# Performance work log

Hardware: AMD Instinct MI355X
Metric: run time of the kernel (lower is better)

The kernel has to match this reference:

```python
import jax, jax.numpy as jnp
import numpy as np

L = 16384      # number of nodes / target positions
N = 1          # batch (graph batches are folded into one graph)
E = 512        # embed_dim
H = 8          # num_heads
D = E // H     # head_dim
DEG = 16       # avg in-degree per query node
NNZ = L * DEG  # number of edges


def setup_inputs() -> dict:
    key = jax.random.key(0)
    ks = jax.random.split(key, 8)
    query = jax.random.normal(ks[0], (L, N, E), dtype=jnp.float32)
    k_in = jax.random.normal(ks[1], (L, N, E), dtype=jnp.float32)
    v_in = jax.random.normal(ks[2], (L, N, E), dtype=jnp.float32)
    # edge list: each query node attends to DEG random source nodes
    row = jnp.repeat(jnp.arange(L, dtype=jnp.int64), DEG)            # (NNZ,)
    col = jax.random.randint(ks[3], (NNZ,), 0, L).astype(jnp.int64)  # (NNZ,)
    indices = jnp.stack([row, col], axis=0)                          # (2, NNZ)
    # parameters (xavier-uniform-like scale)
    in_proj_weight = jax.random.normal(ks[4], (3 * E, E), dtype=jnp.float32) * (1.0 / np.sqrt(E))
    in_proj_bias = jnp.zeros((3 * E,), dtype=jnp.float32)
    out_proj_weight = jax.random.normal(ks[5], (E, E), dtype=jnp.float32) * (1.0 / np.sqrt(E))
    out_proj_bias = jnp.zeros((E,), dtype=jnp.float32)
    return {
        "query": query, "key": k_in, "value": v_in, "indices": indices,
        "in_proj_weight": in_proj_weight, "in_proj_bias": in_proj_bias,
        "out_proj_weight": out_proj_weight, "out_proj_bias": out_proj_bias,
    }


def reference(query, key, value, indices, in_proj_weight, in_proj_bias,
              out_proj_weight, out_proj_bias):
    # QKV projections (in_proj_weight packs [Wq; Wk; Wv] row-wise, torch Linear convention)
    w_q, w_k, w_v = jnp.split(in_proj_weight, 3, axis=0)
    b_q, b_k, b_v = jnp.split(in_proj_bias, 3)
    scaling = 1.0 / jnp.sqrt(jnp.asarray(D, dtype=query.dtype))
    q = (query @ w_q.T + b_q) * scaling          # (L, N, E)
    k = key @ w_k.T + b_k                        # (L, N, E)
    v = value @ w_v.T + b_v                      # (L, N, E)
    # split heads: (L, N*H, D)
    q = q.reshape(L, N * H, D)
    k = k.reshape(L, N * H, D)
    v = v.reshape(L, N * H, D)

    row, col = indices[0], indices[1]
    qe = q[row]                                  # (NNZ, NH, D)
    ke = k[col]                                  # (NNZ, NH, D)
    scores = jnp.einsum('ehd,ehd->eh', qe, ke)   # (NNZ, NH)

    # segment softmax over each query node's edge set
    smax = jax.ops.segment_max(scores, row, num_segments=L)          # (L, NH)
    smax = jnp.where(jnp.isfinite(smax), smax, 0.0)                  # empty-segment guard
    expw = jnp.exp(scores - smax[row])                               # (NNZ, NH)
    denom = jax.ops.segment_sum(expw, row, num_segments=L)           # (L, NH)
    denom = jnp.where(denom > 0, denom, 1.0)
    attn = expw / denom[row]                                         # (NNZ, NH)

    # aggregate values along edges
    ve = v[col]                                                      # (NNZ, NH, D)
    out = jax.ops.segment_sum(attn[:, :, None] * ve, row, num_segments=L)  # (L, NH, D)
    out = out.reshape(L, N, E)
    # output projection
    return out @ out_proj_weight.T + out_proj_bias                   # (L, N, E)
```

## Files before the change

kernel.cpp:

```cpp
#include <hip/hip_runtime.h>
#include <math.h>

#define L_NODES 16384
#define EMB 512
#define NHEAD 8
#define HDIM 64
#define DEG 16
#define NNZ_E (L_NODES * DEG)

typedef __attribute__((ext_vector_type(8))) short short8;
typedef __attribute__((ext_vector_type(4))) float f32x4;

__device__ inline short f2bs(float x) {
    union { float f; unsigned u; } c; c.f = x;
    unsigned r = (c.u + 0x7fffu + ((c.u >> 16) & 1u)) >> 16;
    return (short)r;
}

__device__ inline void cv8(const float* __restrict__ s, short* __restrict__ d, int i) {
    float4 a = reinterpret_cast<const float4*>(s)[2 * i];
    float4 b = reinterpret_cast<const float4*>(s)[2 * i + 1];
    short8 o;
    o[0] = f2bs(a.x); o[1] = f2bs(a.y); o[2] = f2bs(a.z); o[3] = f2bs(a.w);
    o[4] = f2bs(b.x); o[5] = f2bs(b.y); o[6] = f2bs(b.z); o[7] = f2bs(b.w);
    reinterpret_cast<short8*>(d)[i] = o;
}

__global__ __launch_bounds__(256) void f2bw(
    const float* __restrict__ w1, short* __restrict__ d1, int n1,
    const float* __restrict__ w2, short* __restrict__ d2, int n2) {
    const int stride = gridDim.x * blockDim.x;
    for (int i = blockIdx.x * blockDim.x + threadIdx.x; i < n1 + n2; i += stride) {
        if (i < n1) cv8(w1, d1, i); else cv8(w2, d2, i - n1);
    }
}

__device__ inline void b2f8(short8 s, float* f) {
    const unsigned* u = reinterpret_cast<const unsigned*>(&s);
#pragma unroll
    for (int j = 0; j < 4; ++j) {
        unsigned lo = u[j] << 16;
        unsigned hi = u[j] & 0xFFFF0000u;
        f[2 * j]     = __builtin_bit_cast(float, lo);
        f[2 * j + 1] = __builtin_bit_cast(float, hi);
    }
}

__device__ inline void gload16(const short* g, short* l) {
    __builtin_amdgcn_global_load_lds(
        (const __attribute__((address_space(1))) unsigned*)g,
        (__attribute__((address_space(3))) unsigned*)l, 16, 0, 0);
}

__device__ inline short8 cvt16(float4 a0, float4 a1) {
    short8 s;
    s[0] = f2bs(a0.x); s[1] = f2bs(a0.y); s[2] = f2bs(a0.z); s[3] = f2bs(a0.w);
    s[4] = f2bs(a1.x); s[5] = f2bs(a1.y); s[6] = f2bs(a1.z); s[7] = f2bs(a1.w);
    return s;
}

__device__ inline int swz8(int r) { return ((r >> 1) & 3) | ((r & 1) << 2); }

#define QBM 128
#define QBN 256
#define QBK 64

__global__ __launch_bounds__(512) void gemm_qkv(
    const float* __restrict__ q_in, const float* __restrict__ k_in,
    const float* __restrict__ v_in, const short* __restrict__ wqkv,
    const float* __restrict__ bias_all,
    short* __restrict__ qo, short* __restrict__ ko, short* __restrict__ vo)
{
    __shared__ __align__(16) short As[QBM * QBK];
    __shared__ __align__(16) short Bs[QBN * QBK];

    const int gid   = blockIdx.x;
    const int which = gid >> 8;
    const int inner = gid & 255;

    const float* A    = which == 0 ? q_in : (which == 1 ? k_in : v_in);
    const short* B    = wqkv + which * 262144;
    const float* bias = bias_all + which * 512;
    short*       C    = which == 0 ? qo : (which == 1 ? ko : vo);
    const float scale = which == 0 ? 0.125f : 1.0f;

    const int t    = threadIdx.x;
    const int wid  = t >> 6;
    const int lane = t & 63;

    const int wg = (inner & 7) * 32 + (inner >> 3);
    const int bx = wg & 1;
    const int by = wg >> 1;
    const int row0 = by * QBM;
    const int col0 = bx * QBN;

    const int ar  = t >> 2;
    const int q2  = (t & 3) << 1;
    const int xa  = swz8(ar);
    const int p0  = q2 ^ xa;
    const int p1  = p0 ^ 1;
    const float* Aga = A + (size_t)(row0 + ar) * 512 + q2 * 8;
    short* awp0 = &As[ar * QBK + p0 * 8];
    short* awp1 = &As[ar * QBK + p1 * 8];

    const int brw = t >> 3;
    const int bp  = t & 7;
    const int xb  = swz8(brw & 7);
    const short* Bgb = B + (size_t)(col0 + brw) * 512 + (bp ^ xb) * 8;
    short* Bld = &Bs[(wid * 8) * QBK];

    const int wr = wid >> 2;
    const int wc = wid & 3;

    f32x4 acc[4][4] = {};

    for (int k0 = 0; k0 < 512; k0 += QBK) {
#pragma unroll
        for (int j = 0; j < 4; ++j)
            gload16(Bgb + (size_t)j * 64 * 512 + k0, Bld + j * 64 * QBK);
        {
            const float* ap = Aga + k0;
            float4 a0 = *reinterpret_cast<const float4*>(ap);
            float4 a1 = *reinterpret_cast<const float4*>(ap + 4);
            float4 a2 = *reinterpret_cast<const float4*>(ap + 8);
            float4 a3 = *reinterpret_cast<const float4*>(ap + 12);
            *reinterpret_cast<short8*>(awp0) = cvt16(a0, a1);
            *reinterpret_cast<short8*>(awp1) = cvt16(a2, a3);
        }
        __syncthreads();

#pragma unroll
        for (int kk = 0; kk < 2; ++kk) {
            short8 af[4], bf[4];
#pragma unroll
            for (int i = 0; i < 4; ++i) {
                const int r  = wr * 64 + i * 16 + (lane & 15);
                const int sl = (kk * 4 + (lane >> 4)) ^ swz8(r);
                af[i] = *reinterpret_cast<const short8*>(&As[r * QBK + sl * 8]);
            }
#pragma unroll
            for (int j = 0; j < 4; ++j) {
                const int r  = wc * 64 + j * 16 + (lane & 15);
                const int sl = (kk * 4 + (lane >> 4)) ^ swz8(r);
                bf[j] = *reinterpret_cast<const short8*>(&Bs[r * QBK + sl * 8]);
            }
#pragma unroll
            for (int i = 0; i < 4; ++i)
#pragma unroll
                for (int j = 0; j < 4; ++j)
                    acc[i][j] = __builtin_amdgcn_mfma_f32_16x16x32_bf16(
                        af[i], bf[j], acc[i][j], 0, 0, 0);
        }
        __syncthreads();
    }

    float bv[4];
#pragma unroll
    for (int j = 0; j < 4; ++j) bv[j] = bias[col0 + wc * 64 + j * 16 + (lane & 15)];
#pragma unroll
    for (int i = 0; i < 4; ++i) {
        const int rbase = row0 + wr * 64 + i * 16 + (lane >> 4) * 4;
#pragma unroll
        for (int j = 0; j < 4; ++j) {
            const int col = col0 + wc * 64 + j * 16 + (lane & 15);
#pragma unroll
            for (int rg = 0; rg < 4; ++rg)
                C[(size_t)(rbase + rg) * 512 + col] =
                    f2bs((acc[i][j][rg] + bv[j]) * scale);
        }
    }
}

#define OBK 64

__global__ __launch_bounds__(256) void gemm_out(
    const short* __restrict__ A, const short* __restrict__ B,
    const float* __restrict__ bias, float* __restrict__ C)
{
    __shared__ __align__(16) short As[128 * OBK];
    __shared__ __align__(16) short Bs[128 * OBK];

    const int t    = threadIdx.x;
    const int wid  = t >> 6;
    const int lane = t & 63;

    const int cpx = gridDim.x >> 3;
    const int bid = blockIdx.x;
    const int wg  = (bid & 7) * cpx + (bid >> 3);
    const int bx  = wg & 3;
    const int by  = wg >> 2;
    const int row0 = by * 128;
    const int col0 = bx * 128;

    const int rw = t >> 3;
    const int p  = t & 7;
    const int xs = swz8(rw & 7);
    const short* AgS = A + (size_t)(row0 + rw) * 512 + (p ^ xs) * 8;
    const short* BgS = B + (size_t)(col0 + rw) * 512 + (p ^ xs) * 8;
    short* Ald = &As[(wid * 8) * OBK];
    short* Bld = &Bs[(wid * 8) * OBK];

    const int wr = wid >> 1, wc = wid & 1;

    f32x4 acc[4][4] = {};

    for (int k0 = 0; k0 < 512; k0 += OBK) {
#pragma unroll
        for (int j = 0; j < 4; ++j) {
            gload16(AgS + (size_t)j * 32 * 512 + k0, Ald + j * 32 * OBK);
            gload16(BgS + (size_t)j * 32 * 512 + k0, Bld + j * 32 * OBK);
        }
        __syncthreads();

#pragma unroll
        for (int kk = 0; kk < 2; ++kk) {
            short8 af[4], bf[4];
#pragma unroll
            for (int i = 0; i < 4; ++i) {
                const int r  = wr * 64 + i * 16 + (lane & 15);
                const int sl = (kk * 4 + (lane >> 4)) ^ swz8(r);
                af[i] = *reinterpret_cast<const short8*>(&As[r * OBK + sl * 8]);
            }
#pragma unroll
            for (int j = 0; j < 4; ++j) {
                const int r  = wc * 64 + j * 16 + (lane & 15);
                const int sl = (kk * 4 + (lane >> 4)) ^ swz8(r);
                bf[j] = *reinterpret_cast<const short8*>(&Bs[r * OBK + sl * 8]);
            }
#pragma unroll
            for (int i = 0; i < 4; ++i)
#pragma unroll
                for (int j = 0; j < 4; ++j)
                    acc[i][j] = __builtin_amdgcn_mfma_f32_16x16x32_bf16(
                        af[i], bf[j], acc[i][j], 0, 0, 0);
        }
        __syncthreads();
    }

    float bv[4];
#pragma unroll
    for (int j = 0; j < 4; ++j) bv[j] = bias[col0 + wc * 64 + j * 16 + (lane & 15)];
#pragma unroll
    for (int i = 0; i < 4; ++i) {
        const int rbase = row0 + wr * 64 + i * 16 + (lane >> 4) * 4;
#pragma unroll
        for (int j = 0; j < 4; ++j) {
            const int col = col0 + wc * 64 + j * 16 + (lane & 15);
#pragma unroll
            for (int rg = 0; rg < 4; ++rg)
                C[(size_t)(rbase + rg) * 512 + col] = acc[i][j][rg] + bv[j];
        }
    }
}

__device__ inline float edge_core(const float* qf, short8 k0, short8 k1,
                                  short8 v0, short8 v1, int lane) {
    float kf0[8], kf1[8];
    b2f8(k0, kf0); b2f8(k1, kf1);
    float p0 = 0.f, p1 = 0.f;
#pragma unroll
    for (int j = 0; j < 8; ++j) { p0 += qf[j] * kf0[j]; p1 += qf[j] * kf1[j]; }

    const bool b0 = (lane & 1) != 0;
    float x = b0 ? p0 : p1;
    float r = __shfl_xor(x, 1, 64);
    float s = (b0 ? p1 : p0) + r;
    s += __shfl_xor(s, 2, 64);
    s += __shfl_xor(s, 4, 64);

    float m = s;
    m = fmaxf(m, __shfl_xor(m, 1, 64));
    m = fmaxf(m, __shfl_xor(m, 8, 64));
    m = fmaxf(m, __shfl_xor(m, 16, 64));
    m = fmaxf(m, __shfl_xor(m, 32, 64));
    float w = expf(s - m);
    float den = w;
    den += __shfl_xor(den, 1, 64);
    den += __shfl_xor(den, 8, 64);
    den += __shfl_xor(den, 16, 64);
    den += __shfl_xor(den, 32, 64);
    w *= (1.0f / den);

    const int srcb = lane & 56;
    const float w0 = __shfl(w, srcb, 64);
    const float w1 = __shfl(w, srcb | 1, 64);

    float vf0[8], vf1[8], of[8];
    b2f8(v0, vf0); b2f8(v1, vf1);
#pragma unroll
    for (int j = 0; j < 8; ++j) of[j] = w0 * vf0[j] + w1 * vf1[j];

    const bool b3 = (lane & 8) != 0;
    float o4[4];
#pragma unroll
    for (int j = 0; j < 4; ++j) {
        float send = b3 ? of[j] : of[4 + j];
        float recv = __shfl_xor(send, 8, 64);
        o4[j] = (b3 ? of[4 + j] : of[j]) + recv;
    }
    const bool b4 = (lane & 16) != 0;
    float z0 = __shfl_xor(b4 ? o4[0] : o4[2], 16, 64);
    float z1 = __shfl_xor(b4 ? o4[1] : o4[3], 16, 64);
    float t0 = (b4 ? o4[2] : o4[0]) + z0;
    float t1 = (b4 ? o4[3] : o4[1]) + z1;
    const bool b5 = (lane & 32) != 0;
    float zz = __shfl_xor(b5 ? t0 : t1, 32, 64);
    return (b5 ? t1 : t0) + zz;
}

__global__ __launch_bounds__(512) void edge_attn5(
    const short* __restrict__ qm, const short* __restrict__ km,
    const short* __restrict__ vm, const int* __restrict__ colidx,
    short* __restrict__ outb)
{
    const int h    = blockIdx.x & 7;
    const int grp  = blockIdx.x >> 3;
    const int wid  = threadIdx.x >> 6;
    const int lane = threadIdx.x & 63;
    const int i0   = grp * 16 + wid * 2;
    const int c    = lane & 7;
    const int g    = lane >> 3;

    int creg = 0;
    if (lane < 2 * DEG) creg = colidx[i0 * DEG + lane];
    const int ca0 = __shfl(creg, g, 64);
    const int ca1 = __shfl(creg, g + 8, 64);
    const int cb0 = __shfl(creg, 16 + g, 64);
    const int cb1 = __shfl(creg, 16 + g + 8, 64);

    const size_t dof = (size_t)h * HDIM + 8 * c;
    short8 qA  = *reinterpret_cast<const short8*>(&qm[(size_t)i0 * EMB + dof]);
    short8 qB  = *reinterpret_cast<const short8*>(&qm[(size_t)(i0 + 1) * EMB + dof]);
    short8 kA0 = *reinterpret_cast<const short8*>(&km[(size_t)ca0 * EMB + dof]);
    short8 kA1 = *reinterpret_cast<const short8*>(&km[(size_t)ca1 * EMB + dof]);
    short8 kB0 = *reinterpret_cast<const short8*>(&km[(size_t)cb0 * EMB + dof]);
    short8 kB1 = *reinterpret_cast<const short8*>(&km[(size_t)cb1 * EMB + dof]);
    short8 vA0 = *reinterpret_cast<const short8*>(&vm[(size_t)ca0 * EMB + dof]);
    short8 vA1 = *reinterpret_cast<const short8*>(&vm[(size_t)ca1 * EMB + dof]);
    short8 vB0 = *reinterpret_cast<const short8*>(&vm[(size_t)cb0 * EMB + dof]);
    short8 vB1 = *reinterpret_cast<const short8*>(&vm[(size_t)cb1 * EMB + dof]);

    float qfA[8], qfB[8];
    b2f8(qA, qfA); b2f8(qB, qfB);

    const float oA = edge_core(qfA, kA0, kA1, vA0, vA1, lane);
    const float oB = edge_core(qfB, kB0, kB1, vB0, vB1, lane);

    const int d = 8 * c + ((lane & 8) ? 4 : 0) + ((lane & 16) ? 2 : 0)
                        + ((lane & 32) ? 1 : 0);
    outb[(size_t)i0 * EMB + h * HDIM + d]       = f2bs(oA);
    outb[(size_t)(i0 + 1) * EMB + h * HDIM + d] = f2bs(oB);
}

#define TILE 64
#define BKK 16
#define PAD_LD 68

__global__ __launch_bounds__(256) void gemm_bt(
    const float* __restrict__ A, const float* __restrict__ W,
    const float* __restrict__ bias, float* __restrict__ C,
    int M, int K, int N, float scale)
{
    __shared__ float Asm[BKK][PAD_LD];
    __shared__ float Bsm[BKK][PAD_LD];
    const int t  = threadIdx.x;
    const int tx = t & 15;
    const int ty = t >> 4;
    const int row0 = blockIdx.y * TILE;
    const int col0 = blockIdx.x * TILE;
    const int lr = t >> 2;
    const int lk = (t & 3) << 2;
    const float* Aptr = A + (size_t)(row0 + lr) * K + lk;
    const float* Wptr = W + (size_t)(col0 + lr) * K + lk;
    float acc[4][4] = {};
    for (int k0 = 0; k0 < K; k0 += BKK) {
        float4 a4 = *reinterpret_cast<const float4*>(Aptr + k0);
        float4 b4 = *reinterpret_cast<const float4*>(Wptr + k0);
        Asm[lk + 0][lr] = a4.x; Asm[lk + 1][lr] = a4.y;
        Asm[lk + 2][lr] = a4.z; Asm[lk + 3][lr] = a4.w;
        Bsm[lk + 0][lr] = b4.x; Bsm[lk + 1][lr] = b4.y;
        Bsm[lk + 2][lr] = b4.z; Bsm[lk + 3][lr] = b4.w;
        __syncthreads();
#pragma unroll
        for (int kk = 0; kk < BKK; ++kk) {
            float a[4], b[4];
#pragma unroll
            for (int i2 = 0; i2 < 4; ++i2) a[i2] = Asm[kk][ty * 4 + i2];
#pragma unroll
            for (int j2 = 0; j2 < 4; ++j2) b[j2] = Bsm[kk][tx * 4 + j2];
#pragma unroll
            for (int i2 = 0; i2 < 4; ++i2)
#pragma unroll
                for (int j2 = 0; j2 < 4; ++j2)
                    acc[i2][j2] += a[i2] * b[j2];
        }
        __syncthreads();
    }
#pragma unroll
    for (int i2 = 0; i2 < 4; ++i2) {
        const int r = row0 + ty * 4 + i2;
        float4 o;
        o.x = (acc[i2][0] + bias[col0 + tx * 4 + 0]) * scale;
        o.y = (acc[i2][1] + bias[col0 + tx * 4 + 1]) * scale;
        o.z = (acc[i2][2] + bias[col0 + tx * 4 + 2]) * scale;
        o.w = (acc[i2][3] + bias[col0 + tx * 4 + 3]) * scale;
        *reinterpret_cast<float4*>(&C[(size_t)r * N + col0 + tx * 4]) = o;
    }
}

__global__ __launch_bounds__(512) void edge_attn(
    const float* q, const float* __restrict__ kmat, const float* __restrict__ vmat,
    const int* __restrict__ colidx, float* out)
{
    const int i    = blockIdx.x;
    const int h    = threadIdx.x >> 6;
    const int lane = threadIdx.x & 63;
    const size_t base = (size_t)i * EMB + h * HDIM + lane;

    const float qd = q[base];
    int creg = 0;
    if (lane < DEG) creg = colidx[i * DEG + lane];

    float kr[DEG], vr[DEG];
#pragma unroll
    for (int e = 0; e < DEG; ++e) {
        const int ce = __shfl(creg, e, 64);
        const size_t cb = (size_t)ce * EMB + h * HDIM + lane;
        kr[e] = kmat[cb];
        vr[e] = vmat[cb];
    }
    float s[DEG];
#pragma unroll
    for (int e = 0; e < DEG; ++e) {
        float p = qd * kr[e];
#pragma unroll
        for (int off = 32; off; off >>= 1) p += __shfl_xor(p, off, 64);
        s[e] = p;
    }
    float m = s[0];
#pragma unroll
    for (int e = 1; e < DEG; ++e) m = fmaxf(m, s[e]);
    float denom = 0.f;
#pragma unroll
    for (int e = 0; e < DEG; ++e) { s[e] = expf(s[e] - m); denom += s[e]; }
    const float inv = 1.f / denom;
    float o = 0.f;
#pragma unroll
    for (int e = 0; e < DEG; ++e) o += s[e] * vr[e];
    out[base] = o * inv;
}

extern "C" void kernel_launch(void* const* d_in, const int* in_sizes, int n_in,
                              void* d_out, int out_size, void* d_ws, size_t ws_size,
                              hipStream_t stream) {
    const float* query   = (const float*)d_in[0];
    const float* key_    = (const float*)d_in[1];
    const float* value   = (const float*)d_in[2];
    const int*   indices = (const int*)  d_in[3];
    const float* ipw     = (const float*)d_in[4];
    const float* ipb     = (const float*)d_in[5];
    const float* opw     = (const float*)d_in[6];
    const float* opb     = (const float*)d_in[7];
    float* out = (float*)d_out;

    const size_t NEED = 70000000;

    if (ws_size >= NEED) {
        short* wqkv = (short*)d_ws;
        short* wo   = wqkv + 786432;
        short* qo   = wo + 262144;
        short* ko   = qo + 8388608;
        short* vo   = ko + 8388608;
        short* ab   = vo + 8388608;

        f2bw<<<512, 256, 0, stream>>>(ipw, wqkv, 98304, opw, wo, 32768);
        gemm_qkv<<<768, 512, 0, stream>>>(query, key_, value, wqkv, ipb,
                                          qo, ko, vo);
        edge_attn5<<<L_NODES / 2, 512, 0, stream>>>(qo, ko, vo,
                                                    indices + NNZ_E, ab);
        gemm_out<<<512, 256, 0, stream>>>(ab, wo, opb, out);
    } else {
        float* qbuf = (float*)d_ws;
        float* kbuf = qbuf + (size_t)L_NODES * EMB;
        float* vbuf = kbuf + (size_t)L_NODES * EMB;
        const dim3 gblk(EMB / TILE, L_NODES / TILE);
        const float scaling = 0.125f;
        gemm_bt<<<gblk, 256, 0, stream>>>(query, ipw,                 ipb,         qbuf,
                                          L_NODES, EMB, EMB, scaling);
        gemm_bt<<<gblk, 256, 0, stream>>>(key_,  ipw + 1 * EMB * EMB, ipb + EMB,   kbuf,
                                          L_NODES, EMB, EMB, 1.f);
        gemm_bt<<<gblk, 256, 0, stream>>>(value, ipw + 2 * EMB * EMB, ipb + 2*EMB, vbuf,
                                          L_NODES, EMB, EMB, 1.f);
        edge_attn<<<L_NODES, 512, 0, stream>>>(qbuf, kbuf, vbuf, indices + NNZ_E, qbuf);
        gemm_bt<<<gblk, 256, 0, stream>>>(qbuf, opw, opb, out, L_NODES, EMB, EMB, 1.f);
    }
}
```

Measured before the change: 106.5 us.

## Stream fp32 A tiles straight into LDS and retile QKV GEMM to 128x128

The QKV projection GEMM now copies the fp32 activation tile directly into shared memory with async global-to-LDS loads, using a swizzled layout. Before, each tile was loaded through registers and converted to bf16 before the shared-memory store. Conversion to bf16 now happens when MFMA fragments are read. The block tile shrinks from 128x256 with 512 threads to 128x128 with 256 threads, doubling the grid. This removes register staging and stalls on the load path, but doubles LDS traffic for A and repeats the conversion across the waves that share a row block.

```diff
diff --git a/kernel.cpp b/kernel.cpp
--- a/kernel.cpp
+++ b/kernel.cpp
@@ -46,7 +46,7 @@
     }
 }
 
-__device__ inline void gload16(const short* g, short* l) {
+__device__ inline void gload16(const void* g, void* l) {
     __builtin_amdgcn_global_load_lds(
         (const __attribute__((address_space(1))) unsigned*)g,
         (__attribute__((address_space(3))) unsigned*)l, 16, 0, 0);
@@ -61,22 +61,20 @@
 
 __device__ inline int swz8(int r) { return ((r >> 1) & 3) | ((r & 1) << 2); }
 
-#define QBM 128
-#define QBN 256
 #define QBK 64
 
-__global__ __launch_bounds__(512) void gemm_qkv(
+__global__ __launch_bounds__(256) void gemm_qkv(
     const float* __restrict__ q_in, const float* __restrict__ k_in,
     const float* __restrict__ v_in, const short* __restrict__ wqkv,
     const float* __restrict__ bias_all,
     short* __restrict__ qo, short* __restrict__ ko, short* __restrict__ vo)
 {
-    __shared__ __align__(16) short As[QBM * QBK];
-    __shared__ __align__(16) short Bs[QBN * QBK];
+    __shared__ __align__(16) float Asf[128 * QBK];
+    __shared__ __align__(16) short Bs[128 * QBK];
 
     const int gid   = blockIdx.x;
-    const int which = gid >> 8;
-    const int inner = gid & 255;
+    const int which = gid >> 9;
+    const int inner = gid & 511;
 
     const float* A    = which == 0 ? q_in : (which == 1 ? k_in : v_in);
     const short* B    = wqkv + which * 262144;
@@ -88,45 +86,36 @@
     const int wid  = t >> 6;
     const int lane = t & 63;
 
-    const int wg = (inner & 7) * 32 + (inner >> 3);
-    const int bx = wg & 1;
-    const int by = wg >> 1;
-    const int row0 = by * QBM;
-    const int col0 = bx * QBN;
-
-    const int ar  = t >> 2;
-    const int q2  = (t & 3) << 1;
-    const int xa  = swz8(ar);
-    const int p0  = q2 ^ xa;
-    const int p1  = p0 ^ 1;
-    const float* Aga = A + (size_t)(row0 + ar) * 512 + q2 * 8;
-    short* awp0 = &As[ar * QBK + p0 * 8];
-    short* awp1 = &As[ar * QBK + p1 * 8];
+    const int wg = (inner & 7) * 64 + (inner >> 3);
+    const int bx = wg & 3;
+    const int by = wg >> 2;
+    const int row0 = by * 128;
+    const int col0 = bx * 128;
+
+    const int apos = t & 15;
+    const int arow = t >> 4;
+    const int axa  = swz8(arow & 7);
+    const int alog = (apos & 8) | ((apos ^ axa) & 7);
+    const float* AgS = A + (size_t)(row0 + arow) * 512 + alog * 4;
+    float* Alb = &Asf[(size_t)(wid * 64) * 4];
 
     const int brw = t >> 3;
     const int bp  = t & 7;
-    const int xb  = swz8(brw & 7);
-    const short* Bgb = B + (size_t)(col0 + brw) * 512 + (bp ^ xb) * 8;
-    short* Bld = &Bs[(wid * 8) * QBK];
-
-    const int wr = wid >> 2;
-    const int wc = wid & 3;
+    const int bxa = swz8(brw & 7);
+    const short* BgS = B + (size_t)(col0 + brw) * 512 + (bp ^ bxa) * 8;
+    short* Blb = &Bs[(size_t)(wid * 64) * 8];
+
+    const int wr = wid >> 1, wc = wid & 1;
 
     f32x4 acc[4][4] = {};
 
     for (int k0 = 0; k0 < 512; k0 += QBK) {
 #pragma unroll
+        for (int j = 0; j < 8; ++j)
+            gload16(AgS + (size_t)j * 16 * 512 + k0, Alb + (size_t)j * 256 * 4);
+#pragma unroll
         for (int j = 0; j < 4; ++j)
-            gload16(Bgb + (size_t)j * 64 * 512 + k0, Bld + j * 64 * QBK);
-        {
-            const float* ap = Aga + k0;
-            float4 a0 = *reinterpret_cast<const float4*>(ap);
-            float4 a1 = *reinterpret_cast<const float4*>(ap + 4);
-            float4 a2 = *reinterpret_cast<const float4*>(ap + 8);
-            float4 a3 = *reinterpret_cast<const float4*>(ap + 12);
-            *reinterpret_cast<short8*>(awp0) = cvt16(a0, a1);
-            *reinterpret_cast<short8*>(awp1) = cvt16(a2, a3);
-        }
+            gload16(BgS + (size_t)j * 32 * 512 + k0, Blb + (size_t)j * 256 * 8);
         __syncthreads();
 
 #pragma unroll
@@ -135,8 +124,12 @@
 #pragma unroll
             for (int i = 0; i < 4; ++i) {
                 const int r  = wr * 64 + i * 16 + (lane & 15);
-                const int sl = (kk * 4 + (lane >> 4)) ^ swz8(r);
-                af[i] = *reinterpret_cast<const short8*>(&As[r * QBK + sl * 8]);
+                const int l0 = kk * 8 + (lane >> 4) * 2;
+                const int pa = (l0 & 8) | ((l0 ^ swz8(r)) & 7);
+                const int pb = pa ^ 1;
+                float4 va = *reinterpret_cast<const float4*>(&Asf[r * QBK + pa * 4]);
+                float4 vb = *reinterpret_cast<const float4*>(&Asf[r * QBK + pb * 4]);
+                af[i] = cvt16(va, vb);
             }
 #pragma unroll
             for (int j = 0; j < 4; ++j) {
@@ -474,8 +467,8 @@
         short* ab   = vo + 8388608;
 
         f2bw<<<512, 256, 0, stream>>>(ipw, wqkv, 98304, opw, wo, 32768);
-        gemm_qkv<<<768, 512, 0, stream>>>(query, key_, value, wqkv, ipb,
-                                          qo, ko, vo);
+        gemm_qkv<<<1536, 256, 0, stream>>>(query, key_, value, wqkv, ipb,
+                                           qo, ko, vo);
         edge_attn5<<<L_NODES / 2, 512, 0, stream>>>(qo, ko, vo,
                                                     indices + NNZ_E, ab);
         gemm_out<<<512, 256, 0, stream>>>(ab, wo, opb, out);
```

Measured after the change: 112.5 us. +5.6%, slower.
